# Performance work log

Hardware: AMD Instinct MI355X
Metric: run time of the kernel (lower is better)

The kernel has to match this reference:

```python
import jax, jax.numpy as jnp
import numpy as np

B, S, V, D, H, C, NH = 8, 512, 32000, 768, 768, 9, 8
DH = D // NH


def setup_inputs() -> dict:
    key = jax.random.key(0)
    ks = list(jax.random.split(key, 24))
    it = iter(ks)

    def w(shape, s=0.02):
        return jax.random.normal(next(it), shape, jnp.float32) * s

    return {
        "input_ids": jax.random.randint(next(it), (B, S), 0, V, dtype=jnp.int32),
        "labels": jax.random.randint(next(it), (B, S), 0, C, dtype=jnp.int32),
        "emb_table": w((V, D), 1.0),
        "hw_Wh": w((D, D)),
        "hw_bh": jnp.zeros((D,), jnp.float32),
        "hw_Wt": w((D, D)),
        "hw_bt": jnp.zeros((D,), jnp.float32),
        "in_proj_w": w((3 * D, D)),
        "in_proj_b": jnp.zeros((3 * D,), jnp.float32),
        "out_proj_w": w((D, D)),
        "out_proj_b": jnp.zeros((D,), jnp.float32),
        "lstm0_Wih": w((2, 4 * H, D)),
        "lstm0_Whh": w((2, 4 * H, H)),
        "lstm0_b": jnp.zeros((2, 4 * H), jnp.float32),
        "lstm1_Wih": w((2, 4 * H, 2 * H)),
        "lstm1_Whh": w((2, 4 * H, H)),
        "lstm1_b": jnp.zeros((2, 4 * H), jnp.float32),
        "fc_W": w((C, 2 * H)),
        "fc_b": jnp.zeros((C,), jnp.float32),
        "crf_start": w((C,), 0.1),
        "crf_end": w((C,), 0.1),
        "crf_trans": w((C, C), 0.1),
    }


def _lstm_dir(x, Wih, Whh, b, reverse):
    # x: [B,S,in] -> outputs [B,S,H]; PyTorch gate order i,f,g,o
    xt = x.transpose(1, 0, 2)  # [S,B,in]
    h0 = jnp.zeros((x.shape[0], H), x.dtype)

    def step(carry, xt_):
        h, c = carry
        g = xt_ @ Wih.T + h @ Whh.T + b
        i, f, gg, o = jnp.split(g, 4, axis=-1)
        c = jax.nn.sigmoid(f) * c + jax.nn.sigmoid(i) * jnp.tanh(gg)
        h = jax.nn.sigmoid(o) * jnp.tanh(c)
        return (h, c), h

    _, hs = jax.lax.scan(step, (h0, h0), xt, reverse=reverse)
    return hs.transpose(1, 0, 2)


def _bilstm_layer(x, Wih, Whh, b):
    fwd = _lstm_dir(x, Wih[0], Whh[0], b[0], False)
    bwd = _lstm_dir(x, Wih[1], Whh[1], b[1], True)
    return jnp.concatenate([fwd, bwd], axis=-1)


def _emissions(input_ids, emb_table, hw_Wh, hw_bh, hw_Wt, hw_bt,
               in_proj_w, in_proj_b, out_proj_w, out_proj_b,
               lstm0_Wih, lstm0_Whh, lstm0_b, lstm1_Wih, lstm1_Whh, lstm1_b,
               fc_W, fc_b):
    x = emb_table[input_ids]  # [B,S,D]
    # Highway (1 layer, relu)
    hh = jax.nn.relu(x @ hw_Wh.T + hw_bh)
    t = jax.nn.sigmoid(x @ hw_Wt.T + hw_bt)
    x = t * hh + (1.0 - t) * x
    # Multi-head self-attention
    qkv = x @ in_proj_w.T + in_proj_b
    q, k, v = jnp.split(qkv, 3, axis=-1)
    hd = lambda a: a.reshape(B, S, NH, DH).transpose(0, 2, 1, 3)  # [B,NH,S,DH]
    q, k, v = hd(q), hd(k), hd(v)
    att = jax.nn.softmax(jnp.einsum('bhqd,bhkd->bhqk', q, k) / np.float32(np.sqrt(DH)), axis=-1)
    o = jnp.einsum('bhqk,bhkd->bhqd', att, v).transpose(0, 2, 1, 3).reshape(B, S, D)
    x = o @ out_proj_w.T + out_proj_b
    # 2-layer BiLSTM (inference: dropout off)
    x = _bilstm_layer(x, lstm0_Wih, lstm0_Whh, lstm0_b)
    x = _bilstm_layer(x, lstm1_Wih, lstm1_Whh, lstm1_b)
    return x @ fc_W.T + fc_b  # [B,S,C]


def _crf_nll(emissions, tags, crf_start, crf_end, crf_trans):
    # full mask (labels==-100 replaced by 0 before mask built), reduction='sum'
    em_t = emissions.transpose(1, 0, 2)  # [S,B,C]
    num = crf_start[tags[:, 0]] + crf_end[tags[:, -1]]
    num = num + jnp.take_along_axis(emissions, tags[..., None], axis=-1)[..., 0].sum(-1)
    num = num + crf_trans[tags[:, :-1], tags[:, 1:]].sum(-1)
    a0 = crf_start + em_t[0]  # [B,C]

    def fstep(a, em):
        a = jax.scipy.special.logsumexp(a[:, :, None] + crf_trans[None], axis=1) + em
        return a, None

    aT, _ = jax.lax.scan(fstep, a0, em_t[1:])
    logZ = jax.scipy.special.logsumexp(aT + crf_end, axis=-1)
    return -(num - logZ).sum()


def _viterbi(emissions, crf_start, crf_end, crf_trans):
    em_t = emissions.transpose(1, 0, 2)  # [S,B,C]
    s0 = crf_start + em_t[0]

    def vstep(s, em):
        sc = s[:, :, None] + crf_trans[None]  # [B,C_prev,C_next]
        return jnp.max(sc, axis=1) + em, jnp.argmax(sc, axis=1)

    sT, bps = jax.lax.scan(vstep, s0, em_t[1:])  # bps: [S-1,B,C]
    last = jnp.argmax(sT + crf_end, axis=-1)  # [B]

    def bstep(tag, bp):
        prev = jnp.take_along_axis(bp, tag[:, None], axis=1)[:, 0]
        return prev, prev

    _, path = jax.lax.scan(bstep, last, bps, reverse=True)  # [S-1,B]
    return jnp.concatenate([path, last[None]], axis=0).transpose(1, 0)  # [B,S]


def reference(input_ids, labels, emb_table, hw_Wh, hw_bh, hw_Wt, hw_bt,
              in_proj_w, in_proj_b, out_proj_w, out_proj_b,
              lstm0_Wih, lstm0_Whh, lstm0_b, lstm1_Wih, lstm1_Whh, lstm1_b,
              fc_W, fc_b, crf_start, crf_end, crf_trans):
    emissions = _emissions(input_ids, emb_table, hw_Wh, hw_bh, hw_Wt, hw_bt,
                           in_proj_w, in_proj_b, out_proj_w, out_proj_b,
                           lstm0_Wih, lstm0_Whh, lstm0_b,
                           lstm1_Wih, lstm1_Whh, lstm1_b, fc_W, fc_b)
    loss = _crf_nll(emissions, labels, crf_start, crf_end, crf_trans)
    decode = _viterbi(emissions, crf_start, crf_end, crf_trans)
    return loss, decode
```

## Files before the change

### kernel.cpp

```cpp
#include <hip/hip_runtime.h>
#include <cstdint>

#define B_   8
#define S_   512
#define D_   768
#define C_   9
#define BS_  4096

typedef unsigned long long u64;

__global__ __launch_bounds__(192) void k_embed(const int* __restrict__ ids,
                                               const float* __restrict__ emb,
                                               float* __restrict__ x) {
  int row = blockIdx.x;
  int id = ids[row];
  const float4* src = (const float4*)(emb + (size_t)id * D_);
  float4* dst = (float4*)(x + (size_t)row * D_);
  dst[threadIdx.x] = src[threadIdx.x];
}

#define GIDX(k, m) ((k)*144 + (m) + (((m) >> 5) << 2))

__global__ __launch_bounds__(256) void k_gemm(const float* __restrict__ A,
                                              const float* __restrict__ W,
                                              const float* __restrict__ bias,
                                              float* __restrict__ C,
                                              int M, int N, int K, int act, int mode) {
  __shared__ float As[2][2304];
  __shared__ float Bs[2][2304];
  int bm0 = blockIdx.y * 128, bn0 = blockIdx.x * 128;
  int tid = threadIdx.x;
  int tm = tid >> 4, tn = tid & 15;
  int r0 = tid >> 2, kq = (tid & 3) * 4;
  const float* Aptr = A + (size_t)(bm0 + r0) * K + kq;
  const float* Wptr = W + (size_t)(bn0 + r0) * K + kq;
  const size_t rowK = (size_t)64 * K;

  float acc[8][8];
#pragma unroll
  for (int i = 0; i < 8; ++i)
#pragma unroll
    for (int j = 0; j < 8; ++j) acc[i][j] = 0.f;

#define STAGE(buf, A0, A1, B0, B1)                                           \
  {                                                                          \
    As[buf][GIDX(kq + 0, r0)] = A0.x; As[buf][GIDX(kq + 1, r0)] = A0.y;      \
    As[buf][GIDX(kq + 2, r0)] = A0.z; As[buf][GIDX(kq + 3, r0)] = A0.w;      \
    As[buf][GIDX(kq + 0, r0 + 64)] = A1.x; As[buf][GIDX(kq + 1, r0 + 64)] = A1.y; \
    As[buf][GIDX(kq + 2, r0 + 64)] = A1.z; As[buf][GIDX(kq + 3, r0 + 64)] = A1.w; \
    Bs[buf][GIDX(kq + 0, r0)] = B0.x; Bs[buf][GIDX(kq + 1, r0)] = B0.y;      \
    Bs[buf][GIDX(kq + 2, r0)] = B0.z; Bs[buf][GIDX(kq + 3, r0)] = B0.w;      \
    Bs[buf][GIDX(kq + 0, r0 + 64)] = B1.x; Bs[buf][GIDX(kq + 1, r0 + 64)] = B1.y; \
    Bs[buf][GIDX(kq + 2, r0 + 64)] = B1.z; Bs[buf][GIDX(kq + 3, r0 + 64)] = B1.w; \
  }

  {
    float4 a0 = *(const float4*)(Aptr);
    float4 a1 = *(const float4*)(Aptr + rowK);
    float4 b0 = *(const float4*)(Wptr);
    float4 b1 = *(const float4*)(Wptr + rowK);
    STAGE(0, a0, a1, b0, b1);
  }
  __syncthreads();
  int cur = 0;

  for (int k0 = 0; k0 < K; k0 += 16) {
    bool more = (k0 + 16) < K;
    float4 na0, na1, nb0, nb1;
    if (more) {
      na0 = *(const float4*)(Aptr + k0 + 16);
      na1 = *(const float4*)(Aptr + rowK + k0 + 16);
      nb0 = *(const float4*)(Wptr + k0 + 16);
      nb1 = *(const float4*)(Wptr + rowK + k0 + 16);
    }
#pragma unroll
    for (int kk = 0; kk < 16; ++kk) {
      float a[8], b[8];
      *(float4*)&a[0] = *(const float4*)&As[cur][GIDX(kk, tm * 8)];
      *(float4*)&a[4] = *(const float4*)&As[cur][GIDX(kk, tm * 8 + 4)];
      *(float4*)&b[0] = *(const float4*)&Bs[cur][GIDX(kk, tn * 8)];
      *(float4*)&b[4] = *(const float4*)&Bs[cur][GIDX(kk, tn * 8 + 4)];
#pragma unroll
      for (int i = 0; i < 8; ++i)
#pragma unroll
        for (int j = 0; j < 8; ++j) acc[i][j] += a[i] * b[j];
    }
    if (more) {
      STAGE(cur ^ 1, na0, na1, nb0, nb1);
      __syncthreads();
      cur ^= 1;
    }
  }

  float bv[8];
#pragma unroll
  for (int j = 0; j < 8; ++j) bv[j] = bias[bn0 + tn * 8 + j];
#pragma unroll
  for (int i = 0; i < 8; ++i) {
    int row = bm0 + tm * 8 + i;
    float o[8];
#pragma unroll
    for (int j = 0; j < 8; ++j) {
      float v = acc[i][j] + bv[j];
      if (act == 1) v = fmaxf(v, 0.f);
      else if (act == 2) v = 1.f / (1.f + expf(-v));
      o[j] = v;
    }
    if (mode == 0) {
      float* cp = C + (size_t)row * N + bn0 + tn * 8;
      *(float4*)cp = make_float4(o[0], o[1], o[2], o[3]);
      *(float4*)(cp + 4) = make_float4(o[4], o[5], o[6], o[7]);
    } else {
      int bb = row >> 9, t = row & 511;
#pragma unroll
      for (int j = 0; j < 8; ++j) {
        unsigned n = bn0 + tn * 8 + j;
        unsigned dir = n / 3072u;
        unsigned n2 = n - dir * 3072u;
        unsigned g = n2 / 768u;
        unsigned rem = n2 - g * 768u;
        unsigned grp = rem >> 3, u = rem & 7;
        C[(((size_t)(dir * 512 + t) * 96 + grp) << 8) + u * 32 + g * 8 + bb] = o[j];
      }
    }
  }
}

__global__ __launch_bounds__(256) void k_highway(float* __restrict__ x,
                                                 const float* __restrict__ hh,
                                                 const float* __restrict__ tt) {
  const int n4 = BS_ * D_ / 4;
  for (int i = blockIdx.x * 256 + threadIdx.x; i < n4; i += gridDim.x * 256) {
    float4 xv = ((const float4*)x)[i];
    float4 hv = ((const float4*)hh)[i];
    float4 tv = ((const float4*)tt)[i];
    xv.x = tv.x * hv.x + (1.f - tv.x) * xv.x;
    xv.y = tv.y * hv.y + (1.f - tv.y) * xv.y;
    xv.z = tv.z * hv.z + (1.f - tv.z) * xv.z;
    xv.w = tv.w * hv.w + (1.f - tv.w) * xv.w;
    ((float4*)x)[i] = xv;
  }
}

__global__ __launch_bounds__(256) void k_attn(const float* __restrict__ qkv,
                                              float* __restrict__ out) {
  __shared__ float Qs[16 * 100];
  __shared__ float Ks[32 * 101];
  __shared__ float Ps[16 * 513];
  int bh = blockIdx.x;
  int b = bh >> 3, h = bh & 7;
  int q0 = blockIdx.y * 16;
  int tid = threadIdx.x;
  const float scale = 0.10206207261596577f;

  const float* qb = qkv + (size_t)(b * 512 + q0) * 2304 + h * 96;
  for (int i = tid; i < 16 * 96; i += 256) {
    int r = i / 96, c = i - r * 96;
    Qs[r * 100 + c] = qb[(size_t)r * 2304 + c];
  }
  int qi = tid >> 4, kseg = tid & 15;

  for (int kt = 0; kt < 16; ++kt) {
    __syncthreads();
    const float* kb = qkv + (size_t)(b * 512 + kt * 32) * 2304 + 768 + h * 96;
    for (int i = tid; i < 32 * 96; i += 256) {
      int r = i / 96, c = i - r * 96;
      Ks[r * 101 + c] = kb[(size_t)r * 2304 + c];
    }
    __syncthreads();
    int kj0 = kseg * 2;
    float s0 = 0.f, s1 = 0.f;
    const float* qrow = &Qs[qi * 100];
    const float* k0p = &Ks[kj0 * 101];
    const float* k1p = &Ks[(kj0 + 1) * 101];
#pragma unroll 8
    for (int d = 0; d < 96; ++d) {
      float qv = qrow[d];
      s0 += qv * k0p[d];
      s1 += qv * k1p[d];
    }
    Ps[qi * 513 + kt * 32 + kj0] = s0 * scale;
    Ps[qi * 513 + kt * 32 + kj0 + 1] = s1 * scale;
  }
  __syncthreads();

  {
    float m = -1e30f;
    for (int j = 0; j < 32; ++j) m = fmaxf(m, Ps[qi * 513 + kseg + j * 16]);
    m = fmaxf(m, __shfl_xor(m, 1)); m = fmaxf(m, __shfl_xor(m, 2));
    m = fmaxf(m, __shfl_xor(m, 4)); m = fmaxf(m, __shfl_xor(m, 8));
    float sum = 0.f;
    for (int j = 0; j < 32; ++j) {
      int idx = qi * 513 + kseg + j * 16;
      float e = expf(Ps[idx] - m);
      Ps[idx] = e;
      sum += e;
    }
    sum += __shfl_xor(sum, 1); sum += __shfl_xor(sum, 2);
    sum += __shfl_xor(sum, 4); sum += __shfl_xor(sum, 8);
    float inv = 1.f / sum;
    for (int j = 0; j < 32; ++j) Ps[qi * 513 + kseg + j * 16] *= inv;
  }

  float acc[6] = {0.f, 0.f, 0.f, 0.f, 0.f, 0.f};
  int d0 = kseg * 6;
  for (int kt = 0; kt < 16; ++kt) {
    __syncthreads();
    const float* vb = qkv + (size_t)(b * 512 + kt * 32) * 2304 + 1536 + h * 96;
    for (int i = tid; i < 32 * 96; i += 256) {
      int r = i / 96, c = i - r * 96;
      Ks[r * 101 + c] = vb[(size_t)r * 2304 + c];
    }
    __syncthreads();
#pragma unroll 4
    for (int kj = 0; kj < 32; ++kj) {
      float p = Ps[qi * 513 + kt * 32 + kj];
      const float* vrow = &Ks[kj * 101 + d0];
#pragma unroll
      for (int u = 0; u < 6; ++u) acc[u] += p * vrow[u];
    }
  }
  float* ob = out + (size_t)(b * 512 + q0 + qi) * 768 + h * 96 + d0;
#pragma unroll
  for (int u = 0; u < 6; ++u) ob[u] = acc[u];
}

#define NWGD 96
__global__ __launch_bounds__(256, 1) void k_lstm(const float* __restrict__ gates,
                                                 const float* __restrict__ Whh,
                                                 float* __restrict__ hbuf,
                                                 float* __restrict__ hs,
                                                 int* __restrict__ flags) {
  __shared__ float hlds[8 * 772];
  int tid = threadIdx.x;
  int wg = blockIdx.x;
  int dir = wg / NWGD;
  int grp = wg % NWGD;
  int rg = tid >> 5;
  int ks = tid & 31;

  float4 w4[4][6];
#pragma unroll
  for (int j = 0; j < 4; ++j) {
    const float* wp = Whh + ((size_t)dir * 3072 + j * 768 + grp * 8 + rg) * 768 + ks * 4;
#pragma unroll
    for (int jj = 0; jj < 6; ++jj)
      w4[j][jj] = *(const float4*)(wp + jj * 128);
  }

  float* hb = hbuf + (size_t)dir * 2 * 6144;
  const float* gbase = gates + (size_t)dir * 512 * 24576 + grp * 256 + tid;
  const float* hp = hlds + ks * 4;
  float cst = 0.f;

  for (int step = 0; step < 512; ++step) {
    int t = dir ? (511 - step) : step;
    float gqv = gbase[(size_t)t * 24576];

#pragma unroll
    for (int i = 0; i < 3; ++i) {
      int idx = i * 256 + tid;
      int b2 = idx / 96;
      int kq = (idx - b2 * 96) * 8;
      const u64* src = (const u64*)(hb + (step & 1) * 6144 + b2 * 768 + kq);
      u64 lo  = __hip_atomic_load(src + 0, __ATOMIC_RELAXED, __HIP_MEMORY_SCOPE_AGENT);
      u64 hi  = __hip_atomic_load(src + 1, __ATOMIC_RELAXED, __HIP_MEMORY_SCOPE_AGENT);
      u64 lo2 = __hip_atomic_load(src + 2, __ATOMIC_RELAXED, __HIP_MEMORY_SCOPE_AGENT);
      u64 hi2 = __hip_atomic_load(src + 3, __ATOMIC_RELAXED, __HIP_MEMORY_SCOPE_AGENT);
      float* dst = &hlds[b2 * 772 + kq];
      *(u64*)(dst + 0) = lo;
      *(u64*)(dst + 2) = hi;
      *(u64*)(dst + 4) = lo2;
      *(u64*)(dst + 6) = hi2;
    }
    __syncthreads();

    float v[32];
#pragma unroll
    for (int i = 0; i < 32; ++i) v[i] = 0.f;
#pragma unroll
    for (int jj = 0; jj < 6; ++jj) {
#pragma unroll
      for (int b2 = 0; b2 < 8; ++b2) {
        float4 hv = *(const float4*)(hp + b2 * 772 + jj * 128);
#pragma unroll
        for (int j = 0; j < 4; ++j) {
          float4 w = w4[j][jj];
          v[j * 8 + b2] = fmaf(w.x, hv.x, v[j * 8 + b2]);
          v[j * 8 + b2] = fmaf(w.y, hv.y, v[j * 8 + b2]);
          v[j * 8 + b2] = fmaf(w.z, hv.z, v[j * 8 + b2]);
          v[j * 8 + b2] = fmaf(w.w, hv.w, v[j * 8 + b2]);
        }
      }
    }

    {
      bool hi = (ks & 16) != 0;
#pragma unroll
      for (int i = 0; i < 16; ++i) {
        float keep = hi ? v[i + 16] : v[i];
        float send = hi ? v[i] : v[i + 16];
        v[i] = keep + __shfl_xor(send, 16);
      }
    }
    {
      bool hi = (ks & 8) != 0;
#pragma unroll
      for (int i = 0; i < 8; ++i) {
        float keep = hi ? v[i + 8] : v[i];
        float send = hi ? v[i] : v[i + 8];
        v[i] = keep + __shfl_xor(send, 8);
      }
    }
    {
      bool hi = (ks & 4) != 0;
#pragma unroll
      for (int i = 0; i < 4; ++i) {
        float keep = hi ? v[i + 4] : v[i];
        float send = hi ? v[i] : v[i + 4];
        v[i] = keep + __shfl_xor(send, 4);
      }
    }
    {
      bool hi = (ks & 2) != 0;
#pragma unroll
      for (int i = 0; i < 2; ++i) {
        float keep = hi ? v[i + 2] : v[i];
        float send = hi ? v[i] : v[i + 2];
        v[i] = keep + __shfl_xor(send, 2);
      }
    }
    {
      bool hi = (ks & 1) != 0;
      float keep = hi ? v[1] : v[0];
      float send = hi ? v[0] : v[1];
      v[0] = keep + __shfl_xor(send, 1);
    }

    float gv = v[0] + gqv;
    float gf = __shfl_down(gv, 8);
    float gg = __shfl_down(gv, 16);
    float go = __shfl_down(gv, 24);
    float hnew = 0.f;
    if (ks < 8) {
      float i_ = 1.f / (1.f + expf(-gv));
      float f_ = 1.f / (1.f + expf(-gf));
      float ci = tanhf(gg);
      float o_ = 1.f / (1.f + expf(-go));
      cst = f_ * cst + i_ * ci;
      hnew = o_ * tanhf(cst);
      __hip_atomic_store(hb + (size_t)((step + 1) & 1) * 6144 + ks * 768 + grp * 8 + rg,
                         hnew, __ATOMIC_RELAXED, __HIP_MEMORY_SCOPE_AGENT);
    }

    __syncthreads();
    if (tid == 0)
      __hip_atomic_store(&flags[wg * 32], step + 1, __ATOMIC_RELAXED, __HIP_MEMORY_SCOPE_AGENT);
    if (ks < 8)
      hs[((size_t)(ks * 512 + t)) * 1536 + dir * 768 + grp * 8 + rg] = hnew;
    if (tid < NWGD) {
      const int* fp = &flags[(dir * NWGD + tid) * 32];
      while (__hip_atomic_load(fp, __ATOMIC_RELAXED, __HIP_MEMORY_SCOPE_AGENT) <= step)
        __builtin_amdgcn_s_sleep(2);
    }
    __syncthreads();
  }
}

__global__ __launch_bounds__(256) void k_fc(const float* __restrict__ A,
                                            const float* __restrict__ Wf,
                                            const float* __restrict__ bf,
                                            float* __restrict__ out) {
  __shared__ float Wl[9 * 1536];
  int tid = threadIdx.x;
  for (int i = tid; i < 9 * 1536; i += 256) Wl[i] = Wf[i];
  __syncthreads();
  int lane = tid & 63, wv = tid >> 6;
  int row = blockIdx.x * 4 + wv;
  const float* a = A + (size_t)row * 1536;
  float acc[9];
#pragma unroll
  for (int c = 0; c < 9; ++c) acc[c] = 0.f;
  for (int i = 0; i < 24; ++i) {
    float av = a[lane + i * 64];
#pragma unroll
    for (int c = 0; c < 9; ++c) acc[c] += av * Wl[c * 1536 + lane + i * 64];
  }
#pragma unroll
  for (int c = 0; c < 9; ++c) {
#pragma unroll
    for (int m = 1; m < 64; m <<= 1) acc[c] += __shfl_xor(acc[c], m);
  }
  if (lane == 0) {
#pragma unroll
    for (int c = 0; c < 9; ++c) out[(size_t)row * 9 + c] = acc[c] + bf[c];
  }
}

__global__ __launch_bounds__(512) void k_crf(const float* __restrict__ em,
                                             const int* __restrict__ labels,
                                             const float* __restrict__ cs,
                                             const float* __restrict__ ce,
                                             const float* __restrict__ ct,
                                             float* __restrict__ out) {
  __shared__ float trans_s[81];
  __shared__ unsigned char bps[8][511][12];
  __shared__ float partres[16];
  int tid = threadIdx.x;
  int b = tid >> 6;
  int lane = tid & 63;
  bool act = lane < 9;
  if (tid < 81) trans_s[tid] = ct[tid];
  __syncthreads();

  float tcol[9];
#pragma unroll
  for (int cp = 0; cp < 9; ++cp) tcol[cp] = act ? trans_s[cp * 9 + lane] : 0.f;

  float a_ = -1e30f, v_ = -1e30f;
  if (act) {
    float e0 = em[((size_t)b * 512) * 9 + lane];
    a_ = cs[lane] + e0;
    v_ = a_;
  }

  float e = act ? em[((size_t)b * 512 + 1) * 9 + lane] : 0.f;
  for (int t = 1; t < 512; ++t) {
    float e_nxt = 0.f;
    if (act && t < 511) e_nxt = em[((size_t)b * 512 + t + 1) * 9 + lane];
    float m = -1e30f, vm = -1e30f;
    int bp = 0;
    float xs[9];
#pragma unroll
    for (int cp = 0; cp < 9; ++cp) {
      float ap = __shfl(a_, cp);
      float vp = __shfl(v_, cp);
      float x = ap + tcol[cp];
      xs[cp] = x;
      m = fmaxf(m, x);
      float y = vp + tcol[cp];
      if (y > vm) { vm = y; bp = cp; }
    }
    float ssum = 0.f;
#pragma unroll
    for (int cp = 0; cp < 9; ++cp) ssum += expf(xs[cp] - m);
    if (act) {
      a_ = m + logf(ssum) + e;
      v_ = vm + e;
      bps[b][t - 1][lane] = (unsigned char)bp;
    }
    e = e_nxt;
  }

  float fin = act ? a_ + ce[lane] : -1e30f;
  float vfin = act ? v_ + ce[lane] : -1e30f;
  float m2 = fin;
  m2 = fmaxf(m2, __shfl_xor(m2, 1)); m2 = fmaxf(m2, __shfl_xor(m2, 2));
  m2 = fmaxf(m2, __shfl_xor(m2, 4)); m2 = fmaxf(m2, __shfl_xor(m2, 8));
  float s2 = expf(fin - m2);
  s2 += __shfl_xor(s2, 1); s2 += __shfl_xor(s2, 2);
  s2 += __shfl_xor(s2, 4); s2 += __shfl_xor(s2, 8);
  float logZ = m2 + logf(s2);

  float bv = vfin; int bi = lane;
#pragma unroll
  for (int s = 1; s < 16; s <<= 1) {
    float ov = __shfl_xor(bv, s);
    int oi = __shfl_xor(bi, s);
    if (ov > bv || (ov == bv && oi < bi)) { bv = ov; bi = oi; }
  }

  float np = 0.f;
  for (int t = lane; t < 512; t += 64) {
    int tg = labels[b * 512 + t];
    np += em[((size_t)b * 512 + t) * 9 + tg];
    if (t < 511) np += trans_s[tg * 9 + labels[b * 512 + t + 1]];
  }
#pragma unroll
  for (int s = 1; s < 64; s <<= 1) np += __shfl_xor(np, s);

  if (lane == 0) {
    np += cs[labels[b * 512]] + ce[labels[b * 512 + 511]];
    partres[b] = np;
    partres[8 + b] = logZ;
    out[1 + b * 512 + 511] = (float)bi;
    int tg = bi;
    for (int t = 510; t >= 0; --t) {
      tg = bps[b][t][tg];
      out[1 + b * 512 + t] = (float)tg;
    }
  }
  __syncthreads();
  if (tid == 0) {
    float acc = 0.f;
#pragma unroll
    for (int b2 = 0; b2 < 8; ++b2) acc += partres[b2] - partres[8 + b2];
    out[0] = -acc;
  }
}

extern "C" void kernel_launch(void* const* d_in, const int* in_sizes, int n_in,
                              void* d_out, int out_size, void* d_ws, size_t ws_size,
                              hipStream_t stream) {
  (void)in_sizes; (void)n_in; (void)out_size; (void)ws_size;
  const int*   ids    = (const int*)d_in[0];
  const int*   labels = (const int*)d_in[1];
  const float* emb    = (const float*)d_in[2];
  const float* hwWh   = (const float*)d_in[3];
  const float* hwbh   = (const float*)d_in[4];
  const float* hwWt   = (const float*)d_in[5];
  const float* hwbt   = (const float*)d_in[6];
  const float* ipw    = (const float*)d_in[7];
  const float* ipb    = (const float*)d_in[8];
  const float* opw    = (const float*)d_in[9];
  const float* opb    = (const float*)d_in[10];
  const float* l0Wih  = (const float*)d_in[11];
  const float* l0Whh  = (const float*)d_in[12];
  const float* l0b    = (const float*)d_in[13];
  const float* l1Wih  = (const float*)d_in[14];
  const float* l1Whh  = (const float*)d_in[15];
  const float* l1b    = (const float*)d_in[16];
  const float* fcW    = (const float*)d_in[17];
  const float* fcb    = (const float*)d_in[18];
  const float* cs     = (const float*)d_in[19];
  const float* ce     = (const float*)d_in[20];
  const float* ct     = (const float*)d_in[21];

  float* ws   = (float*)d_ws;
  float* x0   = ws;
  float* gbuf = ws + 3145728;
  float* hh   = gbuf;
  float* tt   = gbuf + 3145728;
  float* qkv  = gbuf + 6291456;
  float* x1   = ws + 28311552;
  float* hs0  = ws + 31457280;
  float* hs1  = ws + 37748736;
  float* em   = ws + 44040192;
  float* hbuf = ws + 44077056;
  int*   flags = (int*)(ws + 44101632);

  dim3 g768(6, 32), g2304(18, 32), g6144(48, 32);

  k_embed<<<BS_, 192, 0, stream>>>(ids, emb, x0);
  k_gemm<<<g768, 256, 0, stream>>>(x0, hwWh, hwbh, hh, BS_, 768, 768, 1, 0);
  k_gemm<<<g768, 256, 0, stream>>>(x0, hwWt, hwbt, tt, BS_, 768, 768, 2, 0);
  k_highway<<<768, 256, 0, stream>>>(x0, hh, tt);
  k_gemm<<<g2304, 256, 0, stream>>>(x0, ipw, ipb, qkv, BS_, 2304, 768, 0, 0);
  k_attn<<<dim3(64, 32), 256, 0, stream>>>(qkv, x0);
  k_gemm<<<g768, 256, 0, stream>>>(x0, opw, opb, x1, BS_, 768, 768, 0, 0);

  k_gemm<<<g6144, 256, 0, stream>>>(x1, l0Wih, l0b, gbuf, BS_, 6144, 768, 0, 1);
  hipMemsetAsync(hbuf, 0, (24576 + 192 * 32) * sizeof(float), stream);
  k_lstm<<<192, 256, 0, stream>>>(gbuf, l0Whh, hbuf, hs0, flags);

  k_gemm<<<g6144, 256, 0, stream>>>(hs0, l1Wih, l1b, gbuf, BS_, 6144, 1536, 0, 1);
  hipMemsetAsync(hbuf, 0, (24576 + 192 * 32) * sizeof(float), stream);
  k_lstm<<<192, 256, 0, stream>>>(gbuf, l1Whh, hbuf, hs1, flags);

  k_fc<<<1024, 256, 0, stream>>>(hs1, fcW, fcb, em);
  k_crf<<<1, 512, 0, stream>>>(em, labels, cs, ce, ct, (float*)d_out);
}
```

Measured before the change: 8.152 ms.

## Halve LSTM workgroup count with 512-thread blocks and simplify GEMM staging

The persistent LSTM kernel now runs 48 workgroups per direction with 512 threads each, where each workgroup covers 16 hidden units instead of 8. The GEMM's gate-output layout is remapped to match. This halves the number of workgroups taking part in the per-step cross-workgroup flag barrier and spreads the h-state reload across more threads, in an attempt to cut the serial per-step synchronisation latency. The GEMM also drops its register-prefetch double buffering and goes back to a single shared buffer with two barriers per k-tile. That loses the overlap of global loads with compute in the large input-projection GEMMs.

```diff
diff --git a/kernel.cpp b/kernel.cpp
--- a/kernel.cpp
+++ b/kernel.cpp
@@ -26,69 +26,43 @@
                                               const float* __restrict__ bias,
                                               float* __restrict__ C,
                                               int M, int N, int K, int act, int mode) {
-  __shared__ float As[2][2304];
-  __shared__ float Bs[2][2304];
+  __shared__ float As[2304];
+  __shared__ float Bs[2304];
   int bm0 = blockIdx.y * 128, bn0 = blockIdx.x * 128;
   int tid = threadIdx.x;
   int tm = tid >> 4, tn = tid & 15;
-  int r0 = tid >> 2, kq = (tid & 3) * 4;
-  const float* Aptr = A + (size_t)(bm0 + r0) * K + kq;
-  const float* Wptr = W + (size_t)(bn0 + r0) * K + kq;
-  const size_t rowK = (size_t)64 * K;
-
   float acc[8][8];
 #pragma unroll
   for (int i = 0; i < 8; ++i)
 #pragma unroll
     for (int j = 0; j < 8; ++j) acc[i][j] = 0.f;
 
-#define STAGE(buf, A0, A1, B0, B1)                                           \
-  {                                                                          \
-    As[buf][GIDX(kq + 0, r0)] = A0.x; As[buf][GIDX(kq + 1, r0)] = A0.y;      \
-    As[buf][GIDX(kq + 2, r0)] = A0.z; As[buf][GIDX(kq + 3, r0)] = A0.w;      \
-    As[buf][GIDX(kq + 0, r0 + 64)] = A1.x; As[buf][GIDX(kq + 1, r0 + 64)] = A1.y; \
-    As[buf][GIDX(kq + 2, r0 + 64)] = A1.z; As[buf][GIDX(kq + 3, r0 + 64)] = A1.w; \
-    Bs[buf][GIDX(kq + 0, r0)] = B0.x; Bs[buf][GIDX(kq + 1, r0)] = B0.y;      \
-    Bs[buf][GIDX(kq + 2, r0)] = B0.z; Bs[buf][GIDX(kq + 3, r0)] = B0.w;      \
-    Bs[buf][GIDX(kq + 0, r0 + 64)] = B1.x; Bs[buf][GIDX(kq + 1, r0 + 64)] = B1.y; \
-    Bs[buf][GIDX(kq + 2, r0 + 64)] = B1.z; Bs[buf][GIDX(kq + 3, r0 + 64)] = B1.w; \
-  }
-
-  {
-    float4 a0 = *(const float4*)(Aptr);
-    float4 a1 = *(const float4*)(Aptr + rowK);
-    float4 b0 = *(const float4*)(Wptr);
-    float4 b1 = *(const float4*)(Wptr + rowK);
-    STAGE(0, a0, a1, b0, b1);
-  }
-  __syncthreads();
-  int cur = 0;
-
   for (int k0 = 0; k0 < K; k0 += 16) {
-    bool more = (k0 + 16) < K;
-    float4 na0, na1, nb0, nb1;
-    if (more) {
-      na0 = *(const float4*)(Aptr + k0 + 16);
-      na1 = *(const float4*)(Aptr + rowK + k0 + 16);
-      nb0 = *(const float4*)(Wptr + k0 + 16);
-      nb1 = *(const float4*)(Wptr + rowK + k0 + 16);
-    }
+    __syncthreads();
+#pragma unroll
+    for (int j = 0; j < 2; ++j) {
+      int f4 = tid + j * 256;
+      int r = f4 >> 2;
+      int kq = (f4 & 3) * 4;
+      float4 va = *(const float4*)(A + (size_t)(bm0 + r) * K + k0 + kq);
+      As[GIDX(kq + 0, r)] = va.x; As[GIDX(kq + 1, r)] = va.y;
+      As[GIDX(kq + 2, r)] = va.z; As[GIDX(kq + 3, r)] = va.w;
+      float4 vb = *(const float4*)(W + (size_t)(bn0 + r) * K + k0 + kq);
+      Bs[GIDX(kq + 0, r)] = vb.x; Bs[GIDX(kq + 1, r)] = vb.y;
+      Bs[GIDX(kq + 2, r)] = vb.z; Bs[GIDX(kq + 3, r)] = vb.w;
+    }
+    __syncthreads();
 #pragma unroll
     for (int kk = 0; kk < 16; ++kk) {
       float a[8], b[8];
-      *(float4*)&a[0] = *(const float4*)&As[cur][GIDX(kk, tm * 8)];
-      *(float4*)&a[4] = *(const float4*)&As[cur][GIDX(kk, tm * 8 + 4)];
-      *(float4*)&b[0] = *(const float4*)&Bs[cur][GIDX(kk, tn * 8)];
-      *(float4*)&b[4] = *(const float4*)&Bs[cur][GIDX(kk, tn * 8 + 4)];
+      *(float4*)&a[0] = *(const float4*)&As[GIDX(kk, tm * 8)];
+      *(float4*)&a[4] = *(const float4*)&As[GIDX(kk, tm * 8 + 4)];
+      *(float4*)&b[0] = *(const float4*)&Bs[GIDX(kk, tn * 8)];
+      *(float4*)&b[4] = *(const float4*)&Bs[GIDX(kk, tn * 8 + 4)];
 #pragma unroll
       for (int i = 0; i < 8; ++i)
 #pragma unroll
         for (int j = 0; j < 8; ++j) acc[i][j] += a[i] * b[j];
-    }
-    if (more) {
-      STAGE(cur ^ 1, na0, na1, nb0, nb1);
-      __syncthreads();
-      cur ^= 1;
     }
   }
 
@@ -119,8 +93,8 @@
         unsigned n2 = n - dir * 3072u;
         unsigned g = n2 / 768u;
         unsigned rem = n2 - g * 768u;
-        unsigned grp = rem >> 3, u = rem & 7;
-        C[(((size_t)(dir * 512 + t) * 96 + grp) << 8) + u * 32 + g * 8 + bb] = o[j];
+        unsigned grp = rem >> 4, rgI = rem & 15;
+        C[(((size_t)(dir * 512 + t) * 48 + grp) << 9) + rgI * 32 + g * 8 + bb] = o[j];
       }
     }
   }
@@ -225,8 +199,8 @@
   for (int u = 0; u < 6; ++u) ob[u] = acc[u];
 }
 
-#define NWGD 96
-__global__ __launch_bounds__(256, 1) void k_lstm(const float* __restrict__ gates,
+#define NWGD 48
+__global__ __launch_bounds__(512, 1) void k_lstm(const float* __restrict__ gates,
                                                  const float* __restrict__ Whh,
                                                  float* __restrict__ hbuf,
                                                  float* __restrict__ hs,
@@ -238,18 +212,19 @@
   int grp = wg % NWGD;
   int rg = tid >> 5;
   int ks = tid & 31;
+  int unit = grp * 16 + rg;
 
   float4 w4[4][6];
 #pragma unroll
   for (int j = 0; j < 4; ++j) {
-    const float* wp = Whh + ((size_t)dir * 3072 + j * 768 + grp * 8 + rg) * 768 + ks * 4;
+    const float* wp = Whh + ((size_t)dir * 3072 + j * 768 + unit) * 768 + ks * 4;
 #pragma unroll
     for (int jj = 0; jj < 6; ++jj)
       w4[j][jj] = *(const float4*)(wp + jj * 128);
   }
 
   float* hb = hbuf + (size_t)dir * 2 * 6144;
-  const float* gbase = gates + (size_t)dir * 512 * 24576 + grp * 256 + tid;
+  const float* gbase = gates + (size_t)dir * 512 * 24576 + grp * 512 + tid;
   const float* hp = hlds + ks * 4;
   float cst = 0.f;
 
@@ -257,21 +232,17 @@
     int t = dir ? (511 - step) : step;
     float gqv = gbase[(size_t)t * 24576];
 
-#pragma unroll
-    for (int i = 0; i < 3; ++i) {
-      int idx = i * 256 + tid;
-      int b2 = idx / 96;
-      int kq = (idx - b2 * 96) * 8;
-      const u64* src = (const u64*)(hb + (step & 1) * 6144 + b2 * 768 + kq);
-      u64 lo  = __hip_atomic_load(src + 0, __ATOMIC_RELAXED, __HIP_MEMORY_SCOPE_AGENT);
-      u64 hi  = __hip_atomic_load(src + 1, __ATOMIC_RELAXED, __HIP_MEMORY_SCOPE_AGENT);
-      u64 lo2 = __hip_atomic_load(src + 2, __ATOMIC_RELAXED, __HIP_MEMORY_SCOPE_AGENT);
-      u64 hi2 = __hip_atomic_load(src + 3, __ATOMIC_RELAXED, __HIP_MEMORY_SCOPE_AGENT);
-      float* dst = &hlds[b2 * 772 + kq];
-      *(u64*)(dst + 0) = lo;
-      *(u64*)(dst + 2) = hi;
-      *(u64*)(dst + 4) = lo2;
-      *(u64*)(dst + 6) = hi2;
+    {
+      const float* hsrc = hb + (step & 1) * 6144;
+#pragma unroll
+      for (int i = 0; i < 6; ++i) {
+        int idx = i * 512 + tid;
+        int b2 = idx / 384;
+        int p2 = idx - b2 * 384;
+        const u64* src = (const u64*)(hsrc + b2 * 768) + p2;
+        u64 v = __hip_atomic_load(src, __ATOMIC_RELAXED, __HIP_MEMORY_SCOPE_AGENT);
+        *(u64*)&hlds[b2 * 772 + p2 * 2] = v;
+      }
     }
     __syncthreads();
 
@@ -349,7 +320,7 @@
       float o_ = 1.f / (1.f + expf(-go));
       cst = f_ * cst + i_ * ci;
       hnew = o_ * tanhf(cst);
-      __hip_atomic_store(hb + (size_t)((step + 1) & 1) * 6144 + ks * 768 + grp * 8 + rg,
+      __hip_atomic_store(hb + (size_t)((step + 1) & 1) * 6144 + ks * 768 + unit,
                          hnew, __ATOMIC_RELAXED, __HIP_MEMORY_SCOPE_AGENT);
     }
 
@@ -357,7 +328,7 @@
     if (tid == 0)
       __hip_atomic_store(&flags[wg * 32], step + 1, __ATOMIC_RELAXED, __HIP_MEMORY_SCOPE_AGENT);
     if (ks < 8)
-      hs[((size_t)(ks * 512 + t)) * 1536 + dir * 768 + grp * 8 + rg] = hnew;
+      hs[((size_t)(ks * 512 + t)) * 1536 + dir * 768 + unit] = hnew;
     if (tid < NWGD) {
       const int* fp = &flags[(dir * NWGD + tid) * 32];
       while (__hip_atomic_load(fp, __ATOMIC_RELAXED, __HIP_MEMORY_SCOPE_AGENT) <= step)
@@ -550,12 +521,12 @@
   k_gemm<<<g768, 256, 0, stream>>>(x0, opw, opb, x1, BS_, 768, 768, 0, 0);
 
   k_gemm<<<g6144, 256, 0, stream>>>(x1, l0Wih, l0b, gbuf, BS_, 6144, 768, 0, 1);
-  hipMemsetAsync(hbuf, 0, (24576 + 192 * 32) * sizeof(float), stream);
-  k_lstm<<<192, 256, 0, stream>>>(gbuf, l0Whh, hbuf, hs0, flags);
+  hipMemsetAsync(hbuf, 0, (24576 + 96 * 32) * sizeof(float), stream);
+  k_lstm<<<96, 512, 0, stream>>>(gbuf, l0Whh, hbuf, hs0, flags);
 
   k_gemm<<<g6144, 256, 0, stream>>>(hs0, l1Wih, l1b, gbuf, BS_, 6144, 1536, 0, 1);
-  hipMemsetAsync(hbuf, 0, (24576 + 192 * 32) * sizeof(float), stream);
-  k_lstm<<<192, 256, 0, stream>>>(gbuf, l1Whh, hbuf, hs1, flags);
+  hipMemsetAsync(hbuf, 0, (24576 + 96 * 32) * sizeof(float), stream);
+  k_lstm<<<96, 512, 0, stream>>>(gbuf, l1Whh, hbuf, hs1, flags);
 
   k_fc<<<1024, 256, 0, stream>>>(hs1, fcW, fcb, em);
   k_crf<<<1, 512, 0, stream>>>(em, labels, cs, ce, ct, (float*)d_out);
```

Measured after the change: 9.409 ms. +15.4%, slower.
